# Optimization experiments

Measured on AMD Instinct MI355X. Metric: run time of the kernel, lower is better.

## Reference

```python
import jax, jax.numpy as jnp
import numpy as np

N_NODES = 100000
N_EDGES = 1600000
IN_C, HID_C, OUT_C = 64, 64, 40


def setup_inputs() -> dict:
    key = jax.random.key(0)
    ks = jax.random.split(key, 8)
    x = jax.random.normal(ks[0], (N_NODES, IN_C), dtype=jnp.float32)
    edge_index = jax.random.randint(ks[1], (2, N_EDGES), 0, N_NODES, dtype=jnp.int32)
    s = 1.0 / np.sqrt(HID_C)
    W1 = jax.random.uniform(ks[2], (IN_C, HID_C), jnp.float32, -s, s)
    b1 = jnp.zeros((HID_C,), jnp.float32)
    Wh = jax.random.uniform(ks[3], (HID_C, HID_C), jnp.float32, -s, s)
    bh = jnp.zeros((HID_C,), jnp.float32)
    W2 = jax.random.uniform(ks[4], (HID_C, OUT_C), jnp.float32, -s, s)
    b2 = jnp.zeros((OUT_C,), jnp.float32)
    return {"x": x, "edge_index": edge_index, "W1": W1, "b1": b1,
            "Wh": Wh, "bh": bh, "W2": W2, "b2": b2}


def reference(x, edge_index, W1, b1, Wh, bh, W2, b2):
    N = x.shape[0]
    loop = jnp.arange(N, dtype=edge_index.dtype)
    # GCN normalization with self-loops: A_hat = D^-1/2 (A + I) D^-1/2
    src = jnp.concatenate([edge_index[0], loop])  # [E + N]
    dst = jnp.concatenate([edge_index[1], loop])
    deg = jax.ops.segment_sum(jnp.ones_like(dst, dtype=x.dtype), dst, num_segments=N)
    dinv = jnp.where(deg > 0, jax.lax.rsqrt(deg), 0.0)
    norm = dinv[src] * dinv[dst]  # [E + N]

    def gcn_conv(h, W, b):
        h = h @ W                              # [N, out]
        msg = h[src] * norm[:, None]           # gather + scale, [E+N, out]
        return jax.ops.segment_sum(msg, dst, num_segments=N) + b

    h = jax.nn.relu(gcn_conv(x, W1, b1))       # conv1 (dropout = identity in eval)
    h = jax.nn.relu(gcn_conv(h, Wh, bh))       # hidden_conv, layer_size=2 -> one pass
    h = gcn_conv(h, W2, b2)                    # conv2
    return jax.nn.log_softmax(h, axis=1)
```

## Files before the change

kernel.cpp:

```cpp
#include <hip/hip_runtime.h>
#include <hip/hip_bf16.h>
#include <math.h>

#define EPT 16
#define BCAP 16384

typedef _Float16 half8 __attribute__((ext_vector_type(8)));
typedef _Float16 half2v __attribute__((ext_vector_type(2)));
typedef float f32x4 __attribute__((ext_vector_type(4)));

__device__ __forceinline__ unsigned short f16r(float f) {
    _Float16 h = (_Float16)f;
    return __builtin_bit_cast(unsigned short, h);
}


__global__ void scat1_kernel(const int* __restrict__ src, const int* __restrict__ dst,
                             int* __restrict__ cntg, unsigned* __restrict__ ebuf, int E) {
    __shared__ int lh[256];
    __shared__ int lbase[256];
    int tid = threadIdx.x;
    lh[tid] = 0;
    __syncthreads();
    int base = blockIdx.x * (256 * EPT);
    for (int k = 0; k < EPT; ++k) {
        int e = base + k * 256 + tid;
        if (e < E) atomicAdd(&lh[dst[e] >> 9], 1);
    }
    __syncthreads();
    if (lh[tid] > 0) lbase[tid] = atomicAdd(&cntg[tid], lh[tid]);
    lh[tid] = 0;
    __syncthreads();
    for (int k = 0; k < EPT; ++k) {
        int e = base + k * 256 + tid;
        if (e < E) {
            int s = src[e], d = dst[e];
            int b = d >> 9;
            int pos = lbase[b] + atomicAdd(&lh[b], 1);
            ebuf[(size_t)b * BCAP + pos] = ((unsigned)s << 9) | (unsigned)(d & 511);
        }
    }
}

__global__ void build_kernel(const unsigned* __restrict__ ebuf, const int* __restrict__ cntg,
                             int* __restrict__ row_ptr, int* __restrict__ col,
                             float* __restrict__ dinv, int N, int E) {
    __shared__ int deg[512];
    __shared__ int sh[256];
    int b = blockIdx.x;
    int tid = threadIdx.x;

    int v = cntg[tid];
    sh[tid] = v;
    __syncthreads();
    int val = v;
    for (int off = 1; off < 256; off <<= 1) {
        int add = 0;
        if (tid >= off) add = sh[tid - off];
        __syncthreads();
        val += add;
        sh[tid] = val;
        __syncthreads();
    }
    int start = (b > 0) ? sh[b - 1] : 0;
    int cnt = cntg[b];
    __syncthreads();

    int nodeBase = b << 9;
    int nn = N - nodeBase;
    if (nn > 512) nn = 512;
    if (nn < 0) nn = 0;
    const unsigned* eb = ebuf + (size_t)b * BCAP;

    deg[tid] = 0;
    deg[tid + 256] = 0;
    __syncthreads();
    for (int j = tid; j < cnt; j += 256) {
        atomicAdd(&deg[eb[j] & 511u], 1);
    }
    __syncthreads();

    int i0 = tid * 2, i1 = i0 + 1;
    int v0 = deg[i0], v1 = deg[i1];
    int tot = v0 + v1;
    sh[tid] = tot;
    __syncthreads();
    int val2 = tot;
    for (int off = 1; off < 256; off <<= 1) {
        int add = 0;
        if (tid >= off) add = sh[tid - off];
        __syncthreads();
        val2 += add;
        sh[tid] = val2;
        __syncthreads();
    }
    int excl = val2 - tot;

    if (i0 < nn) { row_ptr[nodeBase + i0] = start + excl;      dinv[nodeBase + i0] = rsqrtf((float)v0 + 1.0f); }
    if (i1 < nn) { row_ptr[nodeBase + i1] = start + excl + v0; dinv[nodeBase + i1] = rsqrtf((float)v1 + 1.0f); }
    if (b == 0 && tid == 0) row_ptr[N] = E;
    deg[i0] = start + excl;
    deg[i1] = start + excl + v0;
    __syncthreads();

    for (int j = tid; j < cnt; j += 256) {
        unsigned rec = eb[j];
        int pos = atomicAdd(&deg[rec & 511u], 1);
        col[pos] = (int)(rec >> 9);
    }
}


__global__ void cvtpack_kernel(const float* __restrict__ x, unsigned short* __restrict__ xb,
                               int n4, const float* __restrict__ W1, const float* __restrict__ Wh,
                               const float* __restrict__ W2, unsigned short* __restrict__ wp1,
                               unsigned short* __restrict__ wph, unsigned short* __restrict__ wp2) {
    int bid = blockIdx.x;
    if (bid < 16) {
        int i = bid * 256 + threadIdx.x;
        int j = i & 7;
        int lane = (i >> 3) & 63;
        int hh = (i >> 9) & 1;
        int t = i >> 10;
        int k = hh * 32 + (lane >> 4) * 8 + j;
        int cc = t * 16 + (lane & 15);
        wp1[i] = f16r(W1[k * 64 + cc]);
        wph[i] = f16r(Wh[k * 64 + cc]);
        if (t < 3) wp2[i] = f16r(cc < 40 ? W2[k * 40 + cc] : 0.f);
    } else {
        int i = (bid - 16) * 256 + threadIdx.x;
        if (i < n4) {
            float4 v = *(const float4*)(x + (size_t)i * 4);
            ushort4 o;
            o.x = f16r(v.x); o.y = f16r(v.y); o.z = f16r(v.z); o.w = f16r(v.w);
            *(ushort4*)(xb + (size_t)i * 4) = o;
        }
    }
}


__launch_bounds__(256, 8)
__global__ void agg_kernel(const unsigned short* __restrict__ h, const int* __restrict__ row_ptr,
                           const int* __restrict__ col, const float* __restrict__ dinv,
                           unsigned short* __restrict__ aggout, int n) {
    int tid = threadIdx.x;
    int lane = tid & 63;
    int node = blockIdx.x * 4 + (tid >> 6);
    if (node >= n) return;

    int sub = lane >> 3;
    unsigned choff = (lane & 7) * 16u;

    int beg = row_ptr[node];
    int deg = row_ptr[node + 1] - beg;
    float di = dinv[node];
    int total = deg + 1;

    half2v a0 = (half2v)0, a1 = (half2v)0, a2 = (half2v)0, a3 = (half2v)0;

    int base = 0;
    while (base < total) {
        int vi = base + lane;
        int idx = node;
        float dw = 0.f;
        if (vi < deg) {
            idx = col[beg + vi];
            dw = dinv[idx];
        } else if (vi == deg) {
            dw = di;
        }
        int dwp = __builtin_bit_cast(int, __builtin_amdgcn_cvt_pkrtz(dw, dw));
        int cnt = min(total - base, 64);
#pragma unroll
        for (int it = 0; it < 4; ++it) {
            int c0 = it * 16;
            if (c0 >= cnt) break;
            int e0 = c0 + sub;
            int e1 = c0 + 8 + sub;
            int s0 = __shfl(idx, e0);
            int w0 = __shfl(dwp, e0);
            int s1 = __shfl(idx, e1);
            int w1 = __shfl(dwp, e1);
            uint4 u0 = *(const uint4*)((const char*)h + (((unsigned)s0 << 7) + choff));
            uint4 u1 = *(const uint4*)((const char*)h + (((unsigned)s1 << 7) + choff));
            half2v wv0 = __builtin_bit_cast(half2v, w0);
            half2v wv1 = __builtin_bit_cast(half2v, w1);
            a0 += __builtin_bit_cast(half2v, u0.x) * wv0;
            a1 += __builtin_bit_cast(half2v, u0.y) * wv0;
            a2 += __builtin_bit_cast(half2v, u0.z) * wv0;
            a3 += __builtin_bit_cast(half2v, u0.w) * wv0;
            a0 += __builtin_bit_cast(half2v, u1.x) * wv1;
            a1 += __builtin_bit_cast(half2v, u1.y) * wv1;
            a2 += __builtin_bit_cast(half2v, u1.z) * wv1;
            a3 += __builtin_bit_cast(half2v, u1.w) * wv1;
        }
        base += cnt;
    }
#pragma unroll
    for (int off = 8; off <= 32; off <<= 1) {
        a0 += __builtin_bit_cast(half2v, __shfl_xor(__builtin_bit_cast(int, a0), off));
        a1 += __builtin_bit_cast(half2v, __shfl_xor(__builtin_bit_cast(int, a1), off));
        a2 += __builtin_bit_cast(half2v, __shfl_xor(__builtin_bit_cast(int, a2), off));
        a3 += __builtin_bit_cast(half2v, __shfl_xor(__builtin_bit_cast(int, a3), off));
    }

    if (sub == 0) {
        half2v dih = __builtin_bit_cast(half2v, __builtin_amdgcn_cvt_pkrtz(di, di));
        a0 *= dih; a1 *= dih; a2 *= dih; a3 *= dih;
        uint4 o;
        o.x = __builtin_bit_cast(unsigned, a0);
        o.y = __builtin_bit_cast(unsigned, a1);
        o.z = __builtin_bit_cast(unsigned, a2);
        o.w = __builtin_bit_cast(unsigned, a3);
        *(uint4*)((char*)aggout + (((unsigned)node << 7) + choff)) = o;
    }
}


__global__ void gemm_relu_kernel(const unsigned short* __restrict__ A,
                                 const unsigned short* __restrict__ wp,
                                 const float* __restrict__ bias,
                                 unsigned short* __restrict__ out, int nTiles, int n) {
    int wv = blockIdx.x * 4 + (threadIdx.x >> 6);
    int lane = threadIdx.x & 63;
    if (wv >= nTiles) return;
    int q = lane >> 4, c = lane & 15;

    half8 bfrag[4][2];
#pragma unroll
    for (int t = 0; t < 4; ++t)
#pragma unroll
        for (int hh = 0; hh < 2; ++hh)
            bfrag[t][hh] = *(const half8*)(wp + t * 1024 + hh * 512 + lane * 8);
    float bs[4];
#pragma unroll
    for (int t = 0; t < 4; ++t) bs[t] = bias[t * 16 + c];

    int nodeBase = wv * 16;
    const unsigned short* arow = A + (size_t)(nodeBase + c) * 64 + q * 8;
    half8 a0 = *(const half8*)(arow);
    half8 a1 = *(const half8*)(arow + 32);

    f32x4 acc[4];
#pragma unroll
    for (int t = 0; t < 4; ++t) {
        f32x4 z = {0.f, 0.f, 0.f, 0.f};
        z = __builtin_amdgcn_mfma_f32_16x16x32_f16(a0, bfrag[t][0], z, 0, 0, 0);
        z = __builtin_amdgcn_mfma_f32_16x16x32_f16(a1, bfrag[t][1], z, 0, 0, 0);
        acc[t] = z;
    }

#pragma unroll
    for (int r = 0; r < 4; ++r) {
        int node = nodeBase + q * 4 + r;
        if (node < n) {
            unsigned short* orow = out + (size_t)node * 64;
#pragma unroll
            for (int t = 0; t < 4; ++t)
                orow[t * 16 + c] = f16r(fmaxf(acc[t][r] + bs[t], 0.f));
        }
    }
}

__global__ void gemm_lsm_kernel(const unsigned short* __restrict__ A,
                                const unsigned short* __restrict__ wp,
                                const float* __restrict__ bias,
                                float* __restrict__ out, int nTiles, int n) {
    int wv = blockIdx.x * 4 + (threadIdx.x >> 6);
    int lane = threadIdx.x & 63;
    if (wv >= nTiles) return;
    int q = lane >> 4, c = lane & 15;
    bool v2ok = (c < 8);

    half8 bfrag[3][2];
#pragma unroll
    for (int t = 0; t < 3; ++t)
#pragma unroll
        for (int hh = 0; hh < 2; ++hh)
            bfrag[t][hh] = *(const half8*)(wp + t * 1024 + hh * 512 + lane * 8);
    float bs[3];
    bs[0] = bias[c];
    bs[1] = bias[16 + c];
    bs[2] = v2ok ? bias[32 + c] : 0.f;

    int nodeBase = wv * 16;
    const unsigned short* arow = A + (size_t)(nodeBase + c) * 64 + q * 8;
    half8 a0 = *(const half8*)(arow);
    half8 a1 = *(const half8*)(arow + 32);

    f32x4 acc[3];
#pragma unroll
    for (int t = 0; t < 3; ++t) {
        f32x4 z = {0.f, 0.f, 0.f, 0.f};
        z = __builtin_amdgcn_mfma_f32_16x16x32_f16(a0, bfrag[t][0], z, 0, 0, 0);
        z = __builtin_amdgcn_mfma_f32_16x16x32_f16(a1, bfrag[t][1], z, 0, 0, 0);
        acc[t] = z;
    }

#pragma unroll
    for (int r = 0; r < 4; ++r) {
        int node = nodeBase + q * 4 + r;
        if (node < n) {
            float v0 = acc[0][r] + bs[0];
            float v1 = acc[1][r] + bs[1];
            float v2 = v2ok ? (acc[2][r] + bs[2]) : -INFINITY;
            float m = fmaxf(fmaxf(v0, v1), v2);
#pragma unroll
            for (int off = 1; off <= 8; off <<= 1) m = fmaxf(m, __shfl_xor(m, off));
            float s = expf(v0 - m) + expf(v1 - m) + (v2ok ? expf(v2 - m) : 0.f);
#pragma unroll
            for (int off = 1; off <= 8; off <<= 1) s += __shfl_xor(s, off);
            float ls = m + logf(s);
            float* orow = out + (size_t)node * 40;
            orow[c] = v0 - ls;
            orow[16 + c] = v1 - ls;
            if (v2ok) orow[32 + c] = v2 - ls;
        }
    }
}


extern "C" void kernel_launch(void* const* d_in, const int* in_sizes, int n_in,
                              void* d_out, int out_size, void* d_ws, size_t ws_size,
                              hipStream_t stream) {
    const float* x  = (const float*)d_in[0];
    const int* ei   = (const int*)d_in[1];
    const float* W1 = (const float*)d_in[2];
    const float* b1 = (const float*)d_in[3];
    const float* Wh = (const float*)d_in[4];
    const float* bh = (const float*)d_in[5];
    const float* W2 = (const float*)d_in[6];
    const float* b2 = (const float*)d_in[7];
    float* out = (float*)d_out;

    const int N = in_sizes[0] / 64;
    const int E = in_sizes[1] / 2;
    const int nbuk = (N + 511) >> 9;
    const int nTiles = (N + 15) / 16;
    const int Npad = nTiles * 16;

    const int* srcp = ei;
    const int* dstp = ei + E;

    size_t off = 0;
    auto alloc = [&](size_t bytes) {
        size_t o = off;
        off = (off + bytes + 255) & ~(size_t)255;
        return o;
    };
    char* ws = (char*)d_ws;
    int*      cntg    = (int*)(ws + alloc(256 * 4));
    int*      row_ptr = (int*)(ws + alloc((size_t)(N + 1) * 4));
    float*    dinv    = (float*)(ws + alloc((size_t)N * 4));
    int*      col     = (int*)(ws + alloc((size_t)E * 4));
    unsigned* ebuf    = (unsigned*)(ws + alloc((size_t)nbuk * BCAP * 4));
    unsigned short* wp1  = (unsigned short*)(ws + alloc(4096 * 2));
    unsigned short* wph  = (unsigned short*)(ws + alloc(4096 * 2));
    unsigned short* wp2  = (unsigned short*)(ws + alloc(3072 * 2));
    unsigned short* xb   = (unsigned short*)(ws + alloc((size_t)Npad * 64 * 2));
    unsigned short* aggA = (unsigned short*)(ws + alloc((size_t)Npad * 64 * 2));
    unsigned short* gA   = (unsigned short*)(ws + alloc((size_t)Npad * 64 * 2));
    (void)ws_size;

    hipMemsetAsync(cntg, 0, 256 * 4, stream);

    const int ebGrid = (E + 256 * EPT - 1) / (256 * EPT);
    scat1_kernel<<<ebGrid, 256, 0, stream>>>(srcp, dstp, cntg, ebuf, E);
    build_kernel<<<nbuk, 256, 0, stream>>>(ebuf, cntg, row_ptr, col, dinv, N, E);

    const int n4 = N * 64 / 4;
    cvtpack_kernel<<<16 + (n4 + 255) / 256, 256, 0, stream>>>(x, xb, n4, W1, Wh, W2, wp1, wph, wp2);

    const int aggGrid = (N + 3) / 4;
    const int gemmGrid = (nTiles + 3) / 4;

    agg_kernel<<<aggGrid, 256, 0, stream>>>(xb, row_ptr, col, dinv, aggA, N);
    gemm_relu_kernel<<<gemmGrid, 256, 0, stream>>>(aggA, wp1, b1, gA, nTiles, N);
    agg_kernel<<<aggGrid, 256, 0, stream>>>(gA, row_ptr, col, dinv, aggA, N);
    gemm_relu_kernel<<<gemmGrid, 256, 0, stream>>>(aggA, wph, bh, gA, nTiles, N);
    agg_kernel<<<aggGrid, 256, 0, stream>>>(gA, row_ptr, col, dinv, aggA, N);
    gemm_lsm_kernel<<<gemmGrid, 256, 0, stream>>>(aggA, wp2, b2, out, nTiles, N);
}
```

Before: 276.5 us.

## Pre-scale features by source dinv and drop per-edge weight gathers in aggregation

Folds the source-side normalization dinv[src] into the node features: the fp16 conversion of x and the relu GEMM epilogue now multiply each row by its dinv. The aggregation kernel then sums gathered rows unweighted. This removes the per-edge dinv gather, the weight shuffles and the multiplies, and padded lanes point at an all-zero extra row. The scatter kernel also loads src and dst into registers once instead of reading them twice. In exchange, fp16 rounding happens on pre-scaled values and each feature buffer needs one extra zeroed row.

Result: faster. 267.1 us (-3.4%).

```diff
diff --git a/kernel.cpp b/kernel.cpp
--- a/kernel.cpp
+++ b/kernel.cpp
@@ -12,6 +12,9 @@
 __device__ __forceinline__ unsigned short f16r(float f) {
     _Float16 h = (_Float16)f;
     return __builtin_bit_cast(unsigned short, h);
+}
+__device__ __forceinline__ half2v h2(unsigned u) {
+    return __builtin_bit_cast(half2v, u);
 }
 
 
@@ -23,21 +26,27 @@
     lh[tid] = 0;
     __syncthreads();
     int base = blockIdx.x * (256 * EPT);
+    int ds[EPT], ss[EPT];
+#pragma unroll
     for (int k = 0; k < EPT; ++k) {
         int e = base + k * 256 + tid;
-        if (e < E) atomicAdd(&lh[dst[e] >> 9], 1);
+        ds[k] = (e < E) ? dst[e] : -1;
+        ss[k] = (e < E) ? src[e] : 0;
+    }
+#pragma unroll
+    for (int k = 0; k < EPT; ++k) {
+        if (ds[k] >= 0) atomicAdd(&lh[ds[k] >> 9], 1);
     }
     __syncthreads();
     if (lh[tid] > 0) lbase[tid] = atomicAdd(&cntg[tid], lh[tid]);
     lh[tid] = 0;
     __syncthreads();
+#pragma unroll
     for (int k = 0; k < EPT; ++k) {
-        int e = base + k * 256 + tid;
-        if (e < E) {
-            int s = src[e], d = dst[e];
-            int b = d >> 9;
+        if (ds[k] >= 0) {
+            int b = ds[k] >> 9;
             int pos = lbase[b] + atomicAdd(&lh[b], 1);
-            ebuf[(size_t)b * BCAP + pos] = ((unsigned)s << 9) | (unsigned)(d & 511);
+            ebuf[(size_t)b * BCAP + pos] = ((unsigned)ss[k] << 9) | (unsigned)(ds[k] & 511);
         }
     }
 }
@@ -112,7 +121,8 @@
 
 
 __global__ void cvtpack_kernel(const float* __restrict__ x, unsigned short* __restrict__ xb,
-                               int n4, const float* __restrict__ W1, const float* __restrict__ Wh,
+                               int n4, int npad, const float* __restrict__ dinv,
+                               const float* __restrict__ W1, const float* __restrict__ Wh,
                                const float* __restrict__ W2, unsigned short* __restrict__ wp1,
                                unsigned short* __restrict__ wph, unsigned short* __restrict__ wp2) {
     int bid = blockIdx.x;
@@ -128,11 +138,16 @@
         wph[i] = f16r(Wh[k * 64 + cc]);
         if (t < 3) wp2[i] = f16r(cc < 40 ? W2[k * 40 + cc] : 0.f);
     } else {
+        if (bid == 16 && threadIdx.x < 8) {
+            *(uint4*)(xb + (size_t)npad * 64 + threadIdx.x * 8) = make_uint4(0, 0, 0, 0);
+        }
         int i = (bid - 16) * 256 + threadIdx.x;
         if (i < n4) {
+            float dn = dinv[i >> 4];
             float4 v = *(const float4*)(x + (size_t)i * 4);
             ushort4 o;
-            o.x = f16r(v.x); o.y = f16r(v.y); o.z = f16r(v.z); o.w = f16r(v.w);
+            o.x = f16r(v.x * dn); o.y = f16r(v.y * dn);
+            o.z = f16r(v.z * dn); o.w = f16r(v.w * dn);
             *(ushort4*)(xb + (size_t)i * 4) = o;
         }
     }
@@ -142,7 +157,7 @@
 __launch_bounds__(256, 8)
 __global__ void agg_kernel(const unsigned short* __restrict__ h, const int* __restrict__ row_ptr,
                            const int* __restrict__ col, const float* __restrict__ dinv,
-                           unsigned short* __restrict__ aggout, int n) {
+                           unsigned short* __restrict__ aggout, int n, int zrow) {
     int tid = threadIdx.x;
     int lane = tid & 63;
     int node = blockIdx.x * 4 + (tid >> 6);
@@ -161,38 +176,20 @@
     int base = 0;
     while (base < total) {
         int vi = base + lane;
-        int idx = node;
-        float dw = 0.f;
-        if (vi < deg) {
-            idx = col[beg + vi];
-            dw = dinv[idx];
-        } else if (vi == deg) {
-            dw = di;
-        }
-        int dwp = __builtin_bit_cast(int, __builtin_amdgcn_cvt_pkrtz(dw, dw));
+        int idx = zrow;
+        if (vi < deg) idx = col[beg + vi];
+        else if (vi == deg) idx = node;
         int cnt = min(total - base, 64);
 #pragma unroll
         for (int it = 0; it < 4; ++it) {
             int c0 = it * 16;
             if (c0 >= cnt) break;
-            int e0 = c0 + sub;
-            int e1 = c0 + 8 + sub;
-            int s0 = __shfl(idx, e0);
-            int w0 = __shfl(dwp, e0);
-            int s1 = __shfl(idx, e1);
-            int w1 = __shfl(dwp, e1);
+            int s0 = __shfl(idx, c0 + sub);
+            int s1 = __shfl(idx, c0 + 8 + sub);
             uint4 u0 = *(const uint4*)((const char*)h + (((unsigned)s0 << 7) + choff));
             uint4 u1 = *(const uint4*)((const char*)h + (((unsigned)s1 << 7) + choff));
-            half2v wv0 = __builtin_bit_cast(half2v, w0);
-            half2v wv1 = __builtin_bit_cast(half2v, w1);
-            a0 += __builtin_bit_cast(half2v, u0.x) * wv0;
-            a1 += __builtin_bit_cast(half2v, u0.y) * wv0;
-            a2 += __builtin_bit_cast(half2v, u0.z) * wv0;
-            a3 += __builtin_bit_cast(half2v, u0.w) * wv0;
-            a0 += __builtin_bit_cast(half2v, u1.x) * wv1;
-            a1 += __builtin_bit_cast(half2v, u1.y) * wv1;
-            a2 += __builtin_bit_cast(half2v, u1.z) * wv1;
-            a3 += __builtin_bit_cast(half2v, u1.w) * wv1;
+            a0 += h2(u0.x);  a1 += h2(u0.y);  a2 += h2(u0.z);  a3 += h2(u0.w);
+            a0 += h2(u1.x);  a1 += h2(u1.y);  a2 += h2(u1.z);  a3 += h2(u1.w);
         }
         base += cnt;
     }
@@ -220,7 +217,11 @@
 __global__ void gemm_relu_kernel(const unsigned short* __restrict__ A,
                                  const unsigned short* __restrict__ wp,
                                  const float* __restrict__ bias,
-                                 unsigned short* __restrict__ out, int nTiles, int n) {
+                                 const float* __restrict__ dinv,
+                                 unsigned short* __restrict__ out, int nTiles, int n, int zrow) {
+    if (blockIdx.x == 0 && threadIdx.x < 8) {
+        *(uint4*)(out + (size_t)zrow * 64 + threadIdx.x * 8) = make_uint4(0, 0, 0, 0);
+    }
     int wv = blockIdx.x * 4 + (threadIdx.x >> 6);
     int lane = threadIdx.x & 63;
     if (wv >= nTiles) return;
@@ -254,10 +255,11 @@
     for (int r = 0; r < 4; ++r) {
         int node = nodeBase + q * 4 + r;
         if (node < n) {
+            float dn = dinv[node];
             unsigned short* orow = out + (size_t)node * 64;
 #pragma unroll
             for (int t = 0; t < 4; ++t)
-                orow[t * 16 + c] = f16r(fmaxf(acc[t][r] + bs[t], 0.f));
+                orow[t * 16 + c] = f16r(fmaxf(acc[t][r] + bs[t], 0.f) * dn);
         }
     }
 }
@@ -357,9 +359,9 @@
     unsigned short* wp1  = (unsigned short*)(ws + alloc(4096 * 2));
     unsigned short* wph  = (unsigned short*)(ws + alloc(4096 * 2));
     unsigned short* wp2  = (unsigned short*)(ws + alloc(3072 * 2));
-    unsigned short* xb   = (unsigned short*)(ws + alloc((size_t)Npad * 64 * 2));
+    unsigned short* xb   = (unsigned short*)(ws + alloc((size_t)(Npad + 1) * 64 * 2));
     unsigned short* aggA = (unsigned short*)(ws + alloc((size_t)Npad * 64 * 2));
-    unsigned short* gA   = (unsigned short*)(ws + alloc((size_t)Npad * 64 * 2));
+    unsigned short* gA   = (unsigned short*)(ws + alloc((size_t)(Npad + 1) * 64 * 2));
     (void)ws_size;
 
     hipMemsetAsync(cntg, 0, 256 * 4, stream);
@@ -368,16 +370,17 @@
     scat1_kernel<<<ebGrid, 256, 0, stream>>>(srcp, dstp, cntg, ebuf, E);
     build_kernel<<<nbuk, 256, 0, stream>>>(ebuf, cntg, row_ptr, col, dinv, N, E);
 
-    const int n4 = N * 64 / 4;
-    cvtpack_kernel<<<16 + (n4 + 255) / 256, 256, 0, stream>>>(x, xb, n4, W1, Wh, W2, wp1, wph, wp2);
+    const int n4 = N * 16;
+    cvtpack_kernel<<<16 + (n4 + 255) / 256, 256, 0, stream>>>(x, xb, n4, Npad, dinv,
+                                                              W1, Wh, W2, wp1, wph, wp2);
 
     const int aggGrid = (N + 3) / 4;
     const int gemmGrid = (nTiles + 3) / 4;
 
-    agg_kernel<<<aggGrid, 256, 0, stream>>>(xb, row_ptr, col, dinv, aggA, N);
-    gemm_relu_kernel<<<gemmGrid, 256, 0, stream>>>(aggA, wp1, b1, gA, nTiles, N);
-    agg_kernel<<<aggGrid, 256, 0, stream>>>(gA, row_ptr, col, dinv, aggA, N);
-    gemm_relu_kernel<<<gemmGrid, 256, 0, stream>>>(aggA, wph, bh, gA, nTiles, N);
-    agg_kernel<<<aggGrid, 256, 0, stream>>>(gA, row_ptr, col, dinv, aggA, N);
+    agg_kernel<<<aggGrid, 256, 0, stream>>>(xb, row_ptr, col, dinv, aggA, N, Npad);
+    gemm_relu_kernel<<<gemmGrid, 256, 0, stream>>>(aggA, wp1, b1, dinv, gA, nTiles, N, Npad);
+    agg_kernel<<<aggGrid, 256, 0, stream>>>(gA, row_ptr, col, dinv, aggA, N, Npad);
+    gemm_relu_kernel<<<gemmGrid, 256, 0, stream>>>(aggA, wph, bh, dinv, gA, nTiles, N, Npad);
+    agg_kernel<<<aggGrid, 256, 0, stream>>>(gA, row_ptr, col, dinv, aggA, N, Npad);
     gemm_lsm_kernel<<<gemmGrid, 256, 0, stream>>>(aggA, wp2, b2, out, nTiles, N);
 }
```
